# Optimization experiments

Hardware: AMD Instinct MI355X
Metric: run time of the kernel (lower is better)

The kernel has to match this reference:

```python
import jax, jax.numpy as jnp
import numpy as np

T, N, D, FF, H, L, WND = 32, 512, 128, 2048, 8, 2, 8
EPS = 1e-5


def setup_inputs() -> dict:
    key = jax.random.key(0)
    kit = iter(jax.random.split(key, 64))

    def w(shape, scale=0.02):
        return jax.random.normal(next(kit), shape, jnp.float32) * scale

    inp = {"x": jax.random.normal(next(kit), (T, N, D), jnp.float32)}
    # plain transformer encoder (1 layer) params
    inp["enc_in_proj_w"] = w((3 * D, D)); inp["enc_in_proj_b"] = jnp.zeros((3 * D,), jnp.float32)
    inp["enc_out_proj_w"] = w((D, D));    inp["enc_out_proj_b"] = jnp.zeros((D,), jnp.float32)
    inp["enc_lin1_w"] = w((FF, D));       inp["enc_lin1_b"] = jnp.zeros((FF,), jnp.float32)
    inp["enc_lin2_w"] = w((D, FF));       inp["enc_lin2_b"] = jnp.zeros((D,), jnp.float32)
    inp["enc_ln1_w"] = jnp.ones((D,), jnp.float32); inp["enc_ln1_b"] = jnp.zeros((D,), jnp.float32)
    inp["enc_ln2_w"] = jnp.ones((D,), jnp.float32); inp["enc_ln2_b"] = jnp.zeros((D,), jnp.float32)
    # qk transformer encoder (L layers, stacked params)
    inp["qk_in_proj_w"] = w((L, 3 * D, D)); inp["qk_in_proj_b"] = jnp.zeros((L, 3 * D), jnp.float32)
    inp["qk_out_proj_w"] = w((L, D, D));    inp["qk_out_proj_b"] = jnp.zeros((L, D), jnp.float32)
    inp["qk_lin1_w"] = w((L, FF, D));       inp["qk_lin1_b"] = jnp.zeros((L, FF), jnp.float32)
    inp["qk_lin2_w"] = w((L, D, FF));       inp["qk_lin2_b"] = jnp.zeros((L, D), jnp.float32)
    inp["qk_ln1_w"] = jnp.ones((L, D), jnp.float32); inp["qk_ln1_b"] = jnp.zeros((L, D), jnp.float32)
    inp["qk_ln2_w"] = jnp.ones((L, D), jnp.float32); inp["qk_ln2_b"] = jnp.zeros((L, D), jnp.float32)
    # time2vec (SineActivation(1, D))
    inp["t2v_w"] = w((1, D - 1), 1.0); inp["t2v_b"] = w((D - 1,), 1.0)
    inp["t2v_w0"] = w((1, 1), 1.0);    inp["t2v_b0"] = w((1,), 1.0)
    # output head (no bias)
    inp["out_w"] = w((1, D))
    return inp


def _layer_norm(x, g, b):
    m = jnp.mean(x, -1, keepdims=True)
    v = jnp.mean((x - m) ** 2, -1, keepdims=True)
    return (x - m) * jax.lax.rsqrt(v + EPS) * g + b


def _mha(q, k, v, Wi, bi, Wo, bo, mask):
    # q,k,v: [S, B, D] seq-first (torch MultiheadAttention layout)
    S, B, d = q.shape
    dh = d // H
    Wq, Wk, Wv = jnp.split(Wi, 3, axis=0)
    bq, bk, bv = jnp.split(bi, 3, axis=0)
    qh = (q @ Wq.T + bq).reshape(S, B, H, dh)
    kh = (k @ Wk.T + bk).reshape(k.shape[0], B, H, dh)
    vh = (v @ Wv.T + bv).reshape(v.shape[0], B, H, dh)
    scores = jnp.einsum('qbhf,kbhf->bhqk', qh, kh) / np.float32(np.sqrt(dh))
    if mask is not None:
        scores = scores + mask  # additive [S,S] mask broadcast over batch/heads
    a = jax.nn.softmax(scores, axis=-1)
    o = jnp.einsum('bhqk,kbhf->qbhf', a, vh).reshape(S, B, d)
    return o @ Wo.T + bo


def _enc_layer(src, new_v, p, mask):
    # post-LN torch TransformerEncoderLayer (dropout off / eval mode)
    s2 = _mha(src, src, new_v, p['iw'], p['ib'], p['ow'], p['ob'], mask)
    src = _layer_norm(src + s2, p['ln1w'], p['ln1b'])
    h = jax.nn.relu(src @ p['l1w'].T + p['l1b'])
    s2 = h @ p['l2w'].T + p['l2b']
    return _layer_norm(src + s2, p['ln2w'], p['ln2b'])


def _banded_mask():
    # triu(-inf, 1) + triu(-inf, WND).T -> allow i-WND < j <= i
    i = jnp.arange(T)[:, None]
    j = jnp.arange(T)[None, :]
    allowed = (j <= i) & (j > i - WND)
    return jnp.where(allowed, 0.0, -jnp.inf).astype(jnp.float32)


def reference(x, enc_in_proj_w, enc_in_proj_b, enc_out_proj_w, enc_out_proj_b,
              enc_lin1_w, enc_lin1_b, enc_lin2_w, enc_lin2_b,
              enc_ln1_w, enc_ln1_b, enc_ln2_w, enc_ln2_b,
              qk_in_proj_w, qk_in_proj_b, qk_out_proj_w, qk_out_proj_b,
              qk_lin1_w, qk_lin1_b, qk_lin2_w, qk_lin2_b,
              qk_ln1_w, qk_ln1_b, qk_ln2_w, qk_ln2_b,
              t2v_w, t2v_b, t2v_w0, t2v_b0, out_w):
    # 1) plain encoder over the PAIR axis (original transposes before it: seq=N, batch=T)
    xs = jnp.transpose(x, (1, 0, 2))  # [N, T, D]
    p_enc = dict(iw=enc_in_proj_w, ib=enc_in_proj_b, ow=enc_out_proj_w, ob=enc_out_proj_b,
                 l1w=enc_lin1_w, l1b=enc_lin1_b, l2w=enc_lin2_w, l2b=enc_lin2_b,
                 ln1w=enc_ln1_w, ln1b=enc_ln1_b, ln2w=enc_ln2_w, ln2b=enc_ln2_b)
    outs_zs = jnp.transpose(_enc_layer(xs, xs, p_enc, None), (1, 0, 2))  # [T, N, D]
    # 2) time2vec positional signal at tau = 1..T
    tau = jnp.arange(1, T + 1, dtype=jnp.float32)[:, None]  # [T,1]
    t2v = jnp.concatenate([jnp.sin(tau @ t2v_w + t2v_b), tau @ t2v_w0 + t2v_b0], axis=-1)
    out = x + t2v[:, None, :]  # [T, N, D]
    # 3) qk encoder stack with banded causal+window mask, values = outs_zs
    mask = _banded_mask()
    for l in range(L):
        p = dict(iw=qk_in_proj_w[l], ib=qk_in_proj_b[l], ow=qk_out_proj_w[l], ob=qk_out_proj_b[l],
                 l1w=qk_lin1_w[l], l1b=qk_lin1_b[l], l2w=qk_lin2_w[l], l2b=qk_lin2_b[l],
                 ln1w=qk_ln1_w[l], ln1b=qk_ln1_b[l], ln2w=qk_ln2_w[l], ln2b=qk_ln2_b[l])
        out = _enc_layer(out, outs_zs, p, mask)
    return (out @ out_w.T)[..., 0]  # [T, N]
```

## Files before the change

kernel.cpp:

```cpp
#include <hip/hip_runtime.h>
#include <hip/hip_bf16.h>
#include <math.h>

#define TT 32
#define NN 512
#define DD 128
#define FF_ 2048
#define HH 8
#define LL 2
#define WND_ 8
#define TOK (TT*NN)
#define DH 16

typedef __hip_bfloat16 bf16;
typedef __attribute__((ext_vector_type(8))) short bf16x8;
typedef __attribute__((ext_vector_type(4))) float f32x4;

#define GLD_LDS16(gp, lp) __builtin_amdgcn_global_load_lds( \
    (const __attribute__((address_space(1))) unsigned int*)(gp), \
    (__attribute__((address_space(3))) unsigned int*)(lp), 16, 0, 0)

#define MFMA16(a, b, c) __builtin_amdgcn_mfma_f32_16x16x32_bf16((a), (b), (c), 0, 0, 0)

__device__ inline short f2bs(float f) {
    __hip_bfloat16 h = __float2bfloat16(f);
    return *reinterpret_cast<short*>(&h);
}

template<int BM, int BN>
__global__ __launch_bounds__(256) void mfma_gemm(
    const bf16* __restrict__ A, int lda,
    const bf16* __restrict__ W,
    const float* __restrict__ bias,
    bf16* __restrict__ C, int ldc,
    int K, int relu)
{
    constexpr int WM = BM / 2, WN = BN / 2;
    constexpr int FM = WM / 16, FN = WN / 16;
    constexpr int LA = (BM * 64) / (256 * 16);
    constexpr int LB = (BN * 64) / (256 * 16);

    __shared__ bf16 As[BM * 32];
    __shared__ bf16 Bs[BN * 32];

    const int tid  = threadIdx.x;
    const int lane = tid & 63;
    const int wave = tid >> 6;
    const int wm = wave >> 1, wn = wave & 1;
    const int bm = blockIdx.y * BM, bn = blockIdx.x * BN;

    f32x4 acc[FM][FN];
    #pragma unroll
    for (int m = 0; m < FM; m++)
        #pragma unroll
        for (int n = 0; n < FN; n++)
            acc[m][n] = (f32x4){0.f, 0.f, 0.f, 0.f};

    for (int k0 = 0; k0 < K; k0 += 32) {
        #pragma unroll
        for (int i = 0; i < LA; i++) {
            const int o = (tid + i * 256) * 16;
            const int row = o >> 6;
            const int ce  = (o & 63) >> 1;
            GLD_LDS16(A + (size_t)(bm + row) * lda + k0 + ce, (char*)As + o);
        }
        #pragma unroll
        for (int i = 0; i < LB; i++) {
            const int o = (tid + i * 256) * 16;
            const int row = o >> 6;
            const int ce  = (o & 63) >> 1;
            GLD_LDS16(W + (size_t)(bn + row) * K + k0 + ce, (char*)Bs + o);
        }
        __syncthreads();

        bf16x8 af[FM], bfr[FN];
        #pragma unroll
        for (int m = 0; m < FM; m++)
            af[m] = *(const bf16x8*)(As + (wm * WM + m * 16 + (lane & 15)) * 32 + (lane >> 4) * 8);
        #pragma unroll
        for (int n = 0; n < FN; n++)
            bfr[n] = *(const bf16x8*)(Bs + (wn * WN + n * 16 + (lane & 15)) * 32 + (lane >> 4) * 8);
        #pragma unroll
        for (int m = 0; m < FM; m++)
            #pragma unroll
            for (int n = 0; n < FN; n++)
                acc[m][n] = MFMA16(af[m], bfr[n], acc[m][n]);
        __syncthreads();
    }

    #pragma unroll
    for (int n = 0; n < FN; n++) {
        const int col = bn + wn * WN + n * 16 + (lane & 15);
        const float bv = bias[col];
        #pragma unroll
        for (int m = 0; m < FM; m++) {
            #pragma unroll
            for (int r = 0; r < 4; r++) {
                const int row = bm + wm * WM + m * 16 + (lane >> 4) * 4 + r;
                float v = acc[m][n][r] + bv;
                if (relu) v = fmaxf(v, 0.f);
                C[(size_t)row * ldc + col] = __float2bfloat16(v);
            }
        }
    }
}

__global__ __launch_bounds__(256) void mfma_gemm_ln(
    const bf16* __restrict__ A, int lda,
    const bf16* __restrict__ W,
    const float* __restrict__ bias,
    const bf16* __restrict__ R,
    const float* __restrict__ lng, const float* __restrict__ lnb,
    bf16* __restrict__ Y,
    int K)
{
    constexpr int BM = 64, WM = 32, WN = 64, FM = 2, FN = 4;

    __shared__ bf16 As[BM * 32];
    __shared__ bf16 Bs[128 * 32];
    __shared__ float rsum[BM][2];
    __shared__ float rsq[BM][2];

    const int tid  = threadIdx.x;
    const int lane = tid & 63;
    const int wave = tid >> 6;
    const int wm = wave >> 1, wn = wave & 1;
    const int bm = blockIdx.x * BM;

    f32x4 acc[FM][FN];
    #pragma unroll
    for (int m = 0; m < FM; m++)
        #pragma unroll
        for (int n = 0; n < FN; n++)
            acc[m][n] = (f32x4){0.f, 0.f, 0.f, 0.f};

    for (int k0 = 0; k0 < K; k0 += 32) {
        {
            const int o = tid * 16;
            const int row = o >> 6;
            const int ce  = (o & 63) >> 1;
            GLD_LDS16(A + (size_t)(bm + row) * lda + k0 + ce, (char*)As + o);
        }
        #pragma unroll
        for (int i = 0; i < 2; i++) {
            const int o = (tid + i * 256) * 16;
            const int row = o >> 6;
            const int ce  = (o & 63) >> 1;
            GLD_LDS16(W + (size_t)row * K + k0 + ce, (char*)Bs + o);
        }
        __syncthreads();

        bf16x8 af[FM], bfr[FN];
        #pragma unroll
        for (int m = 0; m < FM; m++)
            af[m] = *(const bf16x8*)(As + (wm * WM + m * 16 + (lane & 15)) * 32 + (lane >> 4) * 8);
        #pragma unroll
        for (int n = 0; n < FN; n++)
            bfr[n] = *(const bf16x8*)(Bs + (wn * WN + n * 16 + (lane & 15)) * 32 + (lane >> 4) * 8);
        #pragma unroll
        for (int m = 0; m < FM; m++)
            #pragma unroll
            for (int n = 0; n < FN; n++)
                acc[m][n] = MFMA16(af[m], bfr[n], acc[m][n]);
        __syncthreads();
    }

    #pragma unroll
    for (int n = 0; n < FN; n++) {
        const int col = wn * WN + n * 16 + (lane & 15);
        const float bv = bias[col];
        #pragma unroll
        for (int m = 0; m < FM; m++) {
            #pragma unroll
            for (int r = 0; r < 4; r++) {
                const int rl = wm * WM + m * 16 + (lane >> 4) * 4 + r;
                acc[m][n][r] += bv + __bfloat162float(R[(size_t)(bm + rl) * 128 + col]);
            }
        }
    }

    #pragma unroll
    for (int m = 0; m < FM; m++) {
        #pragma unroll
        for (int r = 0; r < 4; r++) {
            float s = 0.f, q = 0.f;
            #pragma unroll
            for (int n = 0; n < FN; n++) { float v = acc[m][n][r]; s += v; q += v * v; }
            #pragma unroll
            for (int off = 1; off < 16; off <<= 1) {
                s += __shfl_xor(s, off);
                q += __shfl_xor(q, off);
            }
            const int rl = wm * WM + m * 16 + (lane >> 4) * 4 + r;
            if ((lane & 15) == 0) { rsum[rl][wn] = s; rsq[rl][wn] = q; }
        }
    }
    __syncthreads();

    #pragma unroll
    for (int m = 0; m < FM; m++) {
        #pragma unroll
        for (int r = 0; r < 4; r++) {
            const int rl = wm * WM + m * 16 + (lane >> 4) * 4 + r;
            const float S = rsum[rl][0] + rsum[rl][1];
            const float Q = rsq[rl][0] + rsq[rl][1];
            const float mean = S * (1.0f / 128.0f);
            const float var  = Q * (1.0f / 128.0f) - mean * mean;
            const float rstd = rsqrtf(var + 1e-5f);
            #pragma unroll
            for (int n = 0; n < FN; n++) {
                const int col = wn * WN + n * 16 + (lane & 15);
                const float y = (acc[m][n][r] - mean) * rstd * lng[col] + lnb[col];
                Y[(size_t)(bm + rl) * 128 + col] = __float2bfloat16(y);
            }
        }
    }
}

template<bool HEAD>
__global__ __launch_bounds__(512) void ffn_fused(
    const bf16* __restrict__ A,
    const bf16* __restrict__ W1, const float* __restrict__ b1,
    const bf16* __restrict__ W2, const float* __restrict__ b2,
    const float* __restrict__ lng, const float* __restrict__ lnb,
    bf16* __restrict__ Y,
    const float* __restrict__ hw, float* __restrict__ hout)
{
    __shared__ char smem[131072];

    const int tid  = threadIdx.x;
    const int lane = tid & 63;
    const int wv   = tid >> 6;
    const int tg   = wv & 1;
    const int hq   = wv >> 1;
    const int l4   = lane & 15;
    const int g    = lane >> 4;
    const int bm   = blockIdx.x * 64;

    bf16x8 tf[2][4];
    #pragma unroll
    for (int sub = 0; sub < 2; sub++)
        #pragma unroll
        for (int j = 0; j < 4; j++)
            tf[sub][j] = *(const bf16x8*)(A + (size_t)(bm + (tg * 2 + sub) * 16 + l4) * 128
                                          + j * 32 + g * 8);

    const int q    = tid >> 4;
    const int qq   = q & 15;
    const int piq  = (((qq >> 2) << 3) | (qq & 3)) + ((q >> 4) << 2);
    const int w1cb = ((tid & 15) * 16) ^ ((q & 7) << 4);
    const int w2row = tid >> 2;
    const int w2ce  = ((tid & 3) ^ ((w2row >> 1) & 3)) * 8;

    auto STAGE = [&](int d, int s) {
        #pragma unroll
        for (int hx = 0; hx < 4; hx++) {
            const int c0 = hx * 512 + s * 32;
            GLD_LDS16((const char*)W1 + (size_t)(c0 + piq) * 256 + w1cb,
                      smem + d * 32768 + hx * 8192 + tid * 16);
            GLD_LDS16(W2 + (size_t)w2row * 2048 + c0 + w2ce,
                      smem + 65536 + d * 32768 + hx * 8192 + tid * 16);
        }
    };

    f32x4 Oacc[2][8];
    #pragma unroll
    for (int sub = 0; sub < 2; sub++)
        #pragma unroll
        for (int ot = 0; ot < 8; ot++)
            Oacc[sub][ot] = (f32x4){0.f, 0.f, 0.f, 0.f};

    const f32x4 zz = (f32x4){0.f, 0.f, 0.f, 0.f};
    const int xsw = (l4 & 7) << 4;
    const int w2rsw = (l4 >> 1) & 3;

    STAGE(0, 0);
    for (int s = 0; s < 16; s++) {
        __syncthreads();
        if (s < 15) STAGE((s + 1) & 1, s + 1);
        const int d  = s & 1;
        const int c0 = hq * 512 + s * 32;
        const char* w1b = smem + d * 32768 + hq * 8192;
        const char* w2b = smem + 65536 + d * 32768 + hq * 8192;

        f32x4 sa00 = zz, sa01 = zz, sa10 = zz, sa11 = zz;
        #pragma unroll
        for (int j = 0; j < 4; j++) {
            const int xo = (j * 64 + g * 16) ^ xsw;
            bf16x8 w10 = *(const bf16x8*)(w1b + l4 * 256 + xo);
            bf16x8 w11 = *(const bf16x8*)(w1b + (16 + l4) * 256 + xo);
            sa00 = MFMA16(w10, tf[0][j], sa00);
            sa01 = MFMA16(w10, tf[1][j], sa01);
            sa10 = MFMA16(w11, tf[0][j], sa10);
            sa11 = MFMA16(w11, tf[1][j], sa11);
        }
        float4 bv0 = *(const float4*)(b1 + c0 + g * 8);
        float4 bv1 = *(const float4*)(b1 + c0 + g * 8 + 4);
        bf16x8 pf0, pf1;
        pf0[0] = f2bs(fmaxf(sa00[0] + bv0.x, 0.f));
        pf0[1] = f2bs(fmaxf(sa00[1] + bv0.y, 0.f));
        pf0[2] = f2bs(fmaxf(sa00[2] + bv0.z, 0.f));
        pf0[3] = f2bs(fmaxf(sa00[3] + bv0.w, 0.f));
        pf0[4] = f2bs(fmaxf(sa10[0] + bv1.x, 0.f));
        pf0[5] = f2bs(fmaxf(sa10[1] + bv1.y, 0.f));
        pf0[6] = f2bs(fmaxf(sa10[2] + bv1.z, 0.f));
        pf0[7] = f2bs(fmaxf(sa10[3] + bv1.w, 0.f));
        pf1[0] = f2bs(fmaxf(sa01[0] + bv0.x, 0.f));
        pf1[1] = f2bs(fmaxf(sa01[1] + bv0.y, 0.f));
        pf1[2] = f2bs(fmaxf(sa01[2] + bv0.z, 0.f));
        pf1[3] = f2bs(fmaxf(sa01[3] + bv0.w, 0.f));
        pf1[4] = f2bs(fmaxf(sa11[0] + bv1.x, 0.f));
        pf1[5] = f2bs(fmaxf(sa11[1] + bv1.y, 0.f));
        pf1[6] = f2bs(fmaxf(sa11[2] + bv1.z, 0.f));
        pf1[7] = f2bs(fmaxf(sa11[3] + bv1.w, 0.f));

        #pragma unroll
        for (int ot = 0; ot < 8; ot++) {
            bf16x8 w2f = *(const bf16x8*)(w2b + (ot * 16 + l4) * 64 + ((g ^ w2rsw) << 4));
            Oacc[0][ot] = MFMA16(pf0, w2f, Oacc[0][ot]);
            Oacc[1][ot] = MFMA16(pf1, w2f, Oacc[1][ot]);
        }
    }

    __syncthreads();
    if (hq != 0) {
        #pragma unroll
        for (int sub = 0; sub < 2; sub++)
            #pragma unroll
            for (int ot = 0; ot < 8; ot++)
                *(f32x4*)(smem + tg * 49152 + (hq - 1) * 16384 + (sub * 8 + ot) * 1024
                          + lane * 16) = Oacc[sub][ot];
    }
    __syncthreads();
    if (hq == 0) {
        #pragma unroll
        for (int p = 0; p < 3; p++)
            #pragma unroll
            for (int sub = 0; sub < 2; sub++)
                #pragma unroll
                for (int ot = 0; ot < 8; ot++) {
                    f32x4 o2 = *(const f32x4*)(smem + tg * 49152 + p * 16384
                                               + (sub * 8 + ot) * 1024 + lane * 16);
                    Oacc[sub][ot][0] += o2[0]; Oacc[sub][ot][1] += o2[1];
                    Oacc[sub][ot][2] += o2[2]; Oacc[sub][ot][3] += o2[3];
                }

        #pragma unroll
        for (int sub = 0; sub < 2; sub++) {
            float vv[8][4];
            #pragma unroll
            for (int ot = 0; ot < 8; ot++) {
                const int col = ot * 16 + l4;
                const float bv = b2[col];
                #pragma unroll
                for (int r = 0; r < 4; r++) {
                    const int trow = bm + (tg * 2 + sub) * 16 + 4 * g + r;
                    vv[ot][r] = Oacc[sub][ot][r] + bv
                              + __bfloat162float(A[(size_t)trow * 128 + col]);
                }
            }

            #pragma unroll
            for (int r = 0; r < 4; r++) {
                float sm = 0.f, qs = 0.f;
                #pragma unroll
                for (int ot = 0; ot < 8; ot++) { float v = vv[ot][r]; sm += v; qs += v * v; }
                #pragma unroll
                for (int off = 1; off < 16; off <<= 1) {
                    sm += __shfl_xor(sm, off);
                    qs += __shfl_xor(qs, off);
                }
                const float mean = sm * (1.0f / 128.0f);
                const float var  = qs * (1.0f / 128.0f) - mean * mean;
                const float rstd = rsqrtf(var + 1e-5f);
                const int trow = bm + (tg * 2 + sub) * 16 + 4 * g + r;
                float hacc = 0.f;
                #pragma unroll
                for (int ot = 0; ot < 8; ot++) {
                    const int col = ot * 16 + l4;
                    const float y = (vv[ot][r] - mean) * rstd * lng[col] + lnb[col];
                    if (HEAD) hacc += y * hw[col];
                    else Y[(size_t)trow * 128 + col] = __float2bfloat16(y);
                }
                if (HEAD) {
                    #pragma unroll
                    for (int off = 1; off < 16; off <<= 1) hacc += __shfl_xor(hacc, off);
                    if (l4 == 0) hout[trow] = hacc;
                }
            }
        }
    }
}

struct ConvDesc {
    const float *x, *s1, *s2, *s3, *s4, *s5, *s6, *s7, *s8;
    bf16 *dx, *d1, *d2, *d3, *d4, *d5, *d6, *d7, *d8;
    const float *w, *b, *w0, *b0;
    float* tbl;
};

__device__ inline void cvt4(const float* s, bf16* d, int j) {
    float4 v = ((const float4*)s)[j];
    ushort4 o;
    o.x = (unsigned short)f2bs(v.x); o.y = (unsigned short)f2bs(v.y);
    o.z = (unsigned short)f2bs(v.z); o.w = (unsigned short)f2bs(v.w);
    *(ushort4*)((unsigned short*)d + j * 4) = o;
}

#define CP0 524288
#define CP1 536576
#define CP2 540672
#define CP3 606208
#define CP4 671744
#define CP5 696320
#define CP6 704512
#define CP7 835584
#define CP8 966656
#define CP9 967680

__global__ __launch_bounds__(256) void conv_all_kernel(ConvDesc cd)
{
    int i = blockIdx.x * 256 + threadIdx.x;
    if (i < CP0)      cvt4(cd.x,  cd.dx, i);
    else if (i < CP1) cvt4(cd.s1, cd.d1, i - CP0);
    else if (i < CP2) cvt4(cd.s2, cd.d2, i - CP1);
    else if (i < CP3) cvt4(cd.s3, cd.d3, i - CP2);
    else if (i < CP4) cvt4(cd.s4, cd.d4, i - CP3);
    else if (i < CP5) cvt4(cd.s5, cd.d5, i - CP4);
    else if (i < CP6) cvt4(cd.s6, cd.d6, i - CP5);
    else if (i < CP7) cvt4(cd.s7, cd.d7, i - CP6);
    else if (i < CP8) cvt4(cd.s8, cd.d8, i - CP7);
    else if (i < CP9) {
        int e = (i - CP8) * 4;
        int t = e >> 7;
        float tau = (float)(t + 1);
        float4 o;
        #pragma unroll
        for (int k = 0; k < 4; k++) {
            int d = (e + k) & 127;
            ((float*)&o)[k] = (d < 127) ? sinf(tau * cd.w[d] + cd.b[d])
                                        : (tau * cd.w0[0] + cd.b0[0]);
        }
        *(float4*)(cd.tbl + e) = o;
    }
}

__global__ __launch_bounds__(256) void attn_full_mfma(
    const bf16* __restrict__ Qkv, bf16* __restrict__ C)
{
    __shared__ bf16 Qs[512 * 16];
    __shared__ bf16 Ks[512 * 16];
    __shared__ bf16 Vt[16 * 520];
    __shared__ bf16 Zero[32];

    const int t = blockIdx.x >> 3;
    const int h = blockIdx.x & 7;
    const int tid = threadIdx.x;

    if (tid < 32) ((unsigned short*)Zero)[tid] = 0;

    for (int n = tid; n < 512; n += 256) {
        const unsigned short* row = (const unsigned short*)Qkv + (size_t)(t * 512 + n) * 384 + h * 16;
        uint4 q0 = *(const uint4*)(row);
        uint4 q1 = *(const uint4*)(row + 8);
        uint4 k0 = *(const uint4*)(row + 128);
        uint4 k1 = *(const uint4*)(row + 136);
        uint4 v0 = *(const uint4*)(row + 256);
        uint4 v1 = *(const uint4*)(row + 264);
        *(uint4*)((unsigned short*)Qs + n * 16)     = q0;
        *(uint4*)((unsigned short*)Qs + n * 16 + 8) = q1;
        *(uint4*)((unsigned short*)Ks + n * 16)     = k0;
        *(uint4*)((unsigned short*)Ks + n * 16 + 8) = k1;
        union { uint4 u[2]; unsigned short s[16]; } vb;
        vb.u[0] = v0; vb.u[1] = v1;
        #pragma unroll
        for (int f = 0; f < 16; f++)
            ((unsigned short*)Vt)[f * 520 + n] = vb.s[f];
    }
    __syncthreads();

    const int lane = tid & 63;
    const int wv   = tid >> 6;
    const int l4   = lane & 15;
    const int g    = lane >> 4;
    const int qbase = wv * 128;
    const bf16* zp = Zero + (g & 1) * 8;
    const int p0 = ((l4 >> 2) << 3) | (l4 & 3);

    bf16x8 qf[8];
    #pragma unroll
    for (int qt = 0; qt < 8; qt++) {
        const bf16* ap = (g < 2) ? (Qs + (qbase + qt * 16 + l4) * 16 + g * 8) : zp;
        qf[qt] = *(const bf16x8*)ap;
    }

    f32x4 Oacc[8];
    float lsum[8];
    #pragma unroll
    for (int qt = 0; qt < 8; qt++) { Oacc[qt] = (f32x4){0.f,0.f,0.f,0.f}; lsum[qt] = 0.f; }

    const float cexp = 0.25f * 1.44269504088896f;

    for (int kt = 0; kt < 16; kt++) {
        const bf16* k0p = (g < 2) ? (Ks + (kt * 32 + p0)     * 16 + g * 8) : zp;
        const bf16* k1p = (g < 2) ? (Ks + (kt * 32 + p0 + 4) * 16 + g * 8) : zp;
        bf16x8 kf0 = *(const bf16x8*)k0p;
        bf16x8 kf1 = *(const bf16x8*)k1p;
        bf16x8 vf  = *(const bf16x8*)(Vt + l4 * 520 + kt * 32 + g * 8);

        #pragma unroll
        for (int qt = 0; qt < 8; qt++) {
            f32x4 z = (f32x4){0.f,0.f,0.f,0.f};
            f32x4 s0 = MFMA16(kf0, qf[qt], z);
            f32x4 s1 = MFMA16(kf1, qf[qt], z);
            float e[8];
            #pragma unroll
            for (int r = 0; r < 4; r++) {
                e[r]     = exp2f(s0[r] * cexp);
                e[4 + r] = exp2f(s1[r] * cexp);
            }
            lsum[qt] += ((e[0]+e[1])+(e[2]+e[3])) + ((e[4]+e[5])+(e[6]+e[7]));
            bf16x8 pf;
            #pragma unroll
            for (int i = 0; i < 8; i++) pf[i] = f2bs(e[i]);
            Oacc[qt] = MFMA16(pf, vf, Oacc[qt]);
        }
    }

    #pragma unroll
    for (int qt = 0; qt < 8; qt++) {
        float ls = lsum[qt];
        ls += __shfl_xor(ls, 16);
        ls += __shfl_xor(ls, 32);
        #pragma unroll
        for (int r = 0; r < 4; r++) {
            float lq = __shfl(ls, g * 4 + r);
            float o = Oacc[qt][r] / lq;
            int qrow = t * 512 + qbase + qt * 16 + g * 4 + r;
            C[(size_t)qrow * 128 + h * 16 + l4] = __float2bfloat16(o);
        }
    }
}

__global__ __launch_bounds__(256) void attn_banded_kernel(
    const bf16* __restrict__ Qkv, const bf16* __restrict__ Vb, bf16* __restrict__ C)
{
    __shared__ float Qs[TT][129];
    __shared__ float Ksh[TT][129];
    __shared__ float Vs[TT][129];
    const int n = blockIdx.x;
    const int tid = threadIdx.x;

    for (int e = tid; e < TT * DD; e += 256) {
        int t = e >> 7, d = e & 127;
        const bf16* row = Qkv + (size_t)(t * NN + n) * 384;
        Qs[t][d]  = __bfloat162float(row[d]);
        Ksh[t][d] = __bfloat162float(row[128 + d]);
        Vs[t][d]  = __bfloat162float(Vb[(size_t)(t * NN + n) * DD + d]);
    }
    __syncthreads();

    const int h = tid >> 5, i = tid & 31;
    const int hb = h * DH;

    float s[WND_];
    #pragma unroll
    for (int kk = 0; kk < WND_; kk++) {
        int j = i - (WND_ - 1) + kk;
        int jc = j < 0 ? 0 : j;
        float d = 0.f;
        #pragma unroll
        for (int f = 0; f < DH; f++) d += Qs[i][hb + f] * Ksh[jc][hb + f];
        s[kk] = (j >= 0) ? d * 0.25f : -1e30f;
    }
    float m = s[0];
    #pragma unroll
    for (int kk = 1; kk < WND_; kk++) m = fmaxf(m, s[kk]);
    float l = 0.f, p[WND_];
    #pragma unroll
    for (int kk = 0; kk < WND_; kk++) { p[kk] = __expf(s[kk] - m); l += p[kk]; }
    float inv = 1.f / l;
    float acc[DH] = {};
    #pragma unroll
    for (int kk = 0; kk < WND_; kk++) {
        int j = i - (WND_ - 1) + kk;
        int jc = j < 0 ? 0 : j;
        float pw = p[kk] * inv;
        #pragma unroll
        for (int f = 0; f < DH; f++) acc[f] += pw * Vs[jc][hb + f];
    }
    bf16* cp = C + (size_t)(i * NN + n) * DD + hb;
    #pragma unroll
    for (int f = 0; f < DH; f++) cp[f] = __float2bfloat16(acc[f]);
}

__global__ __launch_bounds__(256) void t2v_add_kernel(
    const float* __restrict__ x, const float* __restrict__ tbl, bf16* __restrict__ Y)
{
    int i = blockIdx.x * 256 + threadIdx.x;
    int e = i * 4;
    float4 xv = ((const float4*)x)[i];
    int ti = ((e >> 16) << 7) | (e & 127);
    float4 tv = *(const float4*)(tbl + ti);
    ushort4 o;
    o.x = (unsigned short)f2bs(xv.x + tv.x);
    o.y = (unsigned short)f2bs(xv.y + tv.y);
    o.z = (unsigned short)f2bs(xv.z + tv.z);
    o.w = (unsigned short)f2bs(xv.w + tv.w);
    *(ushort4*)((unsigned short*)Y + e) = o;
}


extern "C" void kernel_launch(void* const* d_in, const int* in_sizes, int n_in,
                              void* d_out, int out_size, void* d_ws, size_t ws_size,
                              hipStream_t stream) {
    const float* x           = (const float*)d_in[0];
    const float* enc_in_w    = (const float*)d_in[1];
    const float* enc_in_b    = (const float*)d_in[2];
    const float* enc_out_w   = (const float*)d_in[3];
    const float* enc_out_b   = (const float*)d_in[4];
    const float* enc_l1w     = (const float*)d_in[5];
    const float* enc_l1b     = (const float*)d_in[6];
    const float* enc_l2w     = (const float*)d_in[7];
    const float* enc_l2b     = (const float*)d_in[8];
    const float* enc_ln1w    = (const float*)d_in[9];
    const float* enc_ln1b    = (const float*)d_in[10];
    const float* enc_ln2w    = (const float*)d_in[11];
    const float* enc_ln2b    = (const float*)d_in[12];
    const float* qk_in_w     = (const float*)d_in[13];
    const float* qk_in_b     = (const float*)d_in[14];
    const float* qk_out_w    = (const float*)d_in[15];
    const float* qk_out_b    = (const float*)d_in[16];
    const float* qk_l1w      = (const float*)d_in[17];
    const float* qk_l1b      = (const float*)d_in[18];
    const float* qk_l2w      = (const float*)d_in[19];
    const float* qk_l2b      = (const float*)d_in[20];
    const float* qk_ln1w     = (const float*)d_in[21];
    const float* qk_ln1b     = (const float*)d_in[22];
    const float* qk_ln2w     = (const float*)d_in[23];
    const float* qk_ln2b     = (const float*)d_in[24];
    const float* t2v_w       = (const float*)d_in[25];
    const float* t2v_b       = (const float*)d_in[26];
    const float* t2v_w0      = (const float*)d_in[27];
    const float* t2v_b0      = (const float*)d_in[28];
    const float* out_w       = (const float*)d_in[29];
    float* out = (float*)d_out;

    char* ws = (char*)d_ws;
    const size_t TOKD = (size_t)TOK * DD;
    size_t off = 0;
    auto alloc = [&](size_t bytes) { char* p = ws + off; off += (bytes + 255) & ~(size_t)255; return p; };

    bf16*  Qb   = (bf16*)alloc((size_t)TOK * 384 * 2);
    bf16*  Vb   = (bf16*)alloc(TOKD * 2);
    bf16*  xb   = (bf16*)alloc(TOKD * 2);
    bf16*  bufA = (bf16*)alloc(TOKD * 2);
    bf16*  Zb   = (bf16*)alloc(TOKD * 2);
    bf16*  Cb   = (bf16*)alloc(TOKD * 2);
    float* t2vt = (float*)alloc((size_t)TT * DD * 4);
    bf16* enc_in_wb  = (bf16*)alloc(384 * DD * 2);
    bf16* enc_out_wb = (bf16*)alloc(DD * DD * 2);
    bf16* enc_l1wb   = (bf16*)alloc((size_t)FF_ * DD * 2);
    bf16* enc_l2wb   = (bf16*)alloc((size_t)DD * FF_ * 2);
    bf16* qk_in_wb   = (bf16*)alloc((size_t)LL * 384 * DD * 2);
    bf16* qk_out_wb  = (bf16*)alloc((size_t)LL * DD * DD * 2);
    bf16* qk_l1wb    = (bf16*)alloc((size_t)LL * FF_ * DD * 2);
    bf16* qk_l2wb    = (bf16*)alloc((size_t)LL * DD * FF_ * 2);

    ConvDesc cd;
    cd.x  = x;        cd.dx = xb;
    cd.s1 = enc_in_w; cd.d1 = enc_in_wb;
    cd.s2 = enc_out_w;cd.d2 = enc_out_wb;
    cd.s3 = enc_l1w;  cd.d3 = enc_l1wb;
    cd.s4 = enc_l2w;  cd.d4 = enc_l2wb;
    cd.s5 = qk_in_w;  cd.d5 = qk_in_wb;
    cd.s6 = qk_out_w; cd.d6 = qk_out_wb;
    cd.s7 = qk_l1w;   cd.d7 = qk_l1wb;
    cd.s8 = qk_l2w;   cd.d8 = qk_l2wb;
    cd.w = t2v_w; cd.b = t2v_b; cd.w0 = t2v_w0; cd.b0 = t2v_b0; cd.tbl = t2vt;
    conv_all_kernel<<<(CP9 + 255) / 256, 256, 0, stream>>>(cd);

    auto gemm128 = [&](const bf16* A, int lda, const bf16* W, const float* bias,
                       bf16* C, int ldc, int M, int N, int K, int relu) {
        dim3 grid(N / 128, M / 128);
        mfma_gemm<128, 128><<<grid, 256, 0, stream>>>(A, lda, W, bias, C, ldc, K, relu);
    };
    auto gemm64 = [&](const bf16* A, int lda, const bf16* W, const float* bias,
                      bf16* C, int ldc, int M, int N, int K, int relu) {
        dim3 grid(N / 64, M / 64);
        mfma_gemm<64, 64><<<grid, 256, 0, stream>>>(A, lda, W, bias, C, ldc, K, relu);
    };
    auto gemm_ln = [&](const bf16* A, int lda, const bf16* W, const float* bias,
                       const bf16* R, const float* lng, const float* lnb,
                       bf16* Y, int M, int K) {
        mfma_gemm_ln<<<M / 64, 256, 0, stream>>>(A, lda, W, bias, R, lng, lnb, Y, K);
    };

    gemm128(xb, DD, enc_in_wb, enc_in_b, Qb, 384, TOK, 384, DD, 0);
    attn_full_mfma<<<TT * HH, 256, 0, stream>>>(Qb, Cb);
    gemm_ln(Cb, DD, enc_out_wb, enc_out_b, xb, enc_ln1w, enc_ln1b, bufA, TOK, DD);
    ffn_fused<false><<<TOK / 64, 512, 0, stream>>>(
        bufA, enc_l1wb, enc_l1b, enc_l2wb, enc_l2b,
        enc_ln2w, enc_ln2b, Zb, nullptr, nullptr);

    t2v_add_kernel<<<(TOK * DD / 4) / 256, 256, 0, stream>>>(x, t2vt, bufA);

    for (int l = 0; l < LL; l++) {
        const bf16* iw   = qk_in_wb  + (size_t)l * 384 * DD;
        const float* ib  = qk_in_b   + (size_t)l * 384;
        const bf16* owt  = qk_out_wb + (size_t)l * DD * DD;
        const float* ob  = qk_out_b  + (size_t)l * DD;
        const bf16* l1w  = qk_l1wb   + (size_t)l * FF_ * DD;
        const float* l1b = qk_l1b    + (size_t)l * FF_;
        const bf16* l2w  = qk_l2wb   + (size_t)l * DD * FF_;
        const float* l2b = qk_l2b    + (size_t)l * DD;

        gemm128(bufA, DD, iw, ib, Qb, 384, TOK, 256, DD, 0);
        gemm64(Zb, DD, iw + (size_t)256 * DD, ib + 256, Vb, DD, TOK, DD, DD, 0);
        attn_banded_kernel<<<NN, 256, 0, stream>>>(Qb, Vb, Cb);
        gemm_ln(Cb, DD, owt, ob, bufA, qk_ln1w + l * DD, qk_ln1b + l * DD, bufA, TOK, DD);
        if (l == LL - 1) {
            ffn_fused<true><<<TOK / 64, 512, 0, stream>>>(
                bufA, l1w, l1b, l2w, l2b,
                qk_ln2w + l * DD, qk_ln2b + l * DD, nullptr, out_w, out);
        } else {
            ffn_fused<false><<<TOK / 64, 512, 0, stream>>>(
                bufA, l1w, l1b, l2w, l2b,
                qk_ln2w + l * DD, qk_ln2b + l * DD, bufA, nullptr, nullptr);
        }
    }
}
```

Before: 222.9 us.

## Fuse QK/V projections into one launch and attention with out-proj+LayerNorm

Merges the Q/K projection and the separate V projection into a single kernel whose third column block reads from the encoder output. It also fuses the banded attention with the output projection, residual add and LayerNorm, so the context stays in swizzled LDS instead of round-tripping through global memory. This removes two kernel launches per layer and the context buffer write and read. The cost is that Wo is read directly from global memory by every block, and the attention blocks now carry more LDS and register pressure.

```diff
diff --git a/kernel.cpp b/kernel.cpp
--- a/kernel.cpp
+++ b/kernel.cpp
@@ -100,6 +100,83 @@
                 float v = acc[m][n][r] + bv;
                 if (relu) v = fmaxf(v, 0.f);
                 C[(size_t)row * ldc + col] = __float2bfloat16(v);
+            }
+        }
+    }
+}
+
+__global__ __launch_bounds__(256) void qkv_proj(
+    const bf16* __restrict__ A1, const bf16* __restrict__ A2,
+    const bf16* __restrict__ W,
+    const float* __restrict__ bias,
+    bf16* __restrict__ Qb, bf16* __restrict__ Vb)
+{
+    constexpr int BM = 128, BN = 128, WM = 64, WN = 64, FM = 4, FN = 4;
+
+    __shared__ bf16 As[BM * 32];
+    __shared__ bf16 Bs[BN * 32];
+
+    const int tid  = threadIdx.x;
+    const int lane = tid & 63;
+    const int wave = tid >> 6;
+    const int wm = wave >> 1, wn = wave & 1;
+    const int bnb = blockIdx.x;
+    const int bm  = blockIdx.y * BM;
+
+    const bf16* A  = (bnb == 2) ? A2 : A1;
+    const bf16* Wb = W + (size_t)bnb * 128 * 128;
+
+    f32x4 acc[FM][FN];
+    #pragma unroll
+    for (int m = 0; m < FM; m++)
+        #pragma unroll
+        for (int n = 0; n < FN; n++)
+            acc[m][n] = (f32x4){0.f, 0.f, 0.f, 0.f};
+
+    for (int k0 = 0; k0 < 128; k0 += 32) {
+        #pragma unroll
+        for (int i = 0; i < 2; i++) {
+            const int o = (tid + i * 256) * 16;
+            const int row = o >> 6;
+            const int ce  = (o & 63) >> 1;
+            GLD_LDS16(A + (size_t)(bm + row) * 128 + k0 + ce, (char*)As + o);
+        }
+        #pragma unroll
+        for (int i = 0; i < 2; i++) {
+            const int o = (tid + i * 256) * 16;
+            const int row = o >> 6;
+            const int ce  = (o & 63) >> 1;
+            GLD_LDS16(Wb + (size_t)row * 128 + k0 + ce, (char*)Bs + o);
+        }
+        __syncthreads();
+
+        bf16x8 af[FM], bfr[FN];
+        #pragma unroll
+        for (int m = 0; m < FM; m++)
+            af[m] = *(const bf16x8*)(As + (wm * WM + m * 16 + (lane & 15)) * 32 + (lane >> 4) * 8);
+        #pragma unroll
+        for (int n = 0; n < FN; n++)
+            bfr[n] = *(const bf16x8*)(Bs + (wn * WN + n * 16 + (lane & 15)) * 32 + (lane >> 4) * 8);
+        #pragma unroll
+        for (int m = 0; m < FM; m++)
+            #pragma unroll
+            for (int n = 0; n < FN; n++)
+                acc[m][n] = MFMA16(af[m], bfr[n], acc[m][n]);
+        __syncthreads();
+    }
+
+    #pragma unroll
+    for (int n = 0; n < FN; n++) {
+        const int cl = wn * WN + n * 16 + (lane & 15);
+        const float bv = bias[bnb * 128 + cl];
+        #pragma unroll
+        for (int m = 0; m < FM; m++) {
+            #pragma unroll
+            for (int r = 0; r < 4; r++) {
+                const int row = bm + wm * WM + m * 16 + (lane >> 4) * 4 + r;
+                const float v = acc[m][n][r] + bv;
+                if (bnb == 2) Vb[(size_t)row * 128 + cl] = __float2bfloat16(v);
+                else          Qb[(size_t)row * 384 + bnb * 128 + cl] = __float2bfloat16(v);
             }
         }
     }
@@ -542,12 +619,22 @@
     }
 }
 
-__global__ __launch_bounds__(256) void attn_banded_kernel(
-    const bf16* __restrict__ Qkv, const bf16* __restrict__ Vb, bf16* __restrict__ C)
+__global__ __launch_bounds__(256) void attn_banded_oln(
+    const bf16* __restrict__ Qkv,
+    const bf16* __restrict__ Vb,
+    const bf16* __restrict__ Wo,
+    const float* __restrict__ ob,
+    const bf16* __restrict__ R,
+    const float* __restrict__ lng, const float* __restrict__ lnb,
+    bf16* __restrict__ Y)
 {
     __shared__ float Qs[TT][129];
     __shared__ float Ksh[TT][129];
     __shared__ float Vs[TT][129];
+    __shared__ bf16 Ctx[32 * 128];
+    __shared__ float rsum[32][2];
+    __shared__ float rsq[32][2];
+
     const int n = blockIdx.x;
     const int tid = threadIdx.x;
 
@@ -560,38 +647,111 @@
     }
     __syncthreads();
 
-    const int h = tid >> 5, i = tid & 31;
-    const int hb = h * DH;
-
-    float s[WND_];
-    #pragma unroll
-    for (int kk = 0; kk < WND_; kk++) {
-        int j = i - (WND_ - 1) + kk;
-        int jc = j < 0 ? 0 : j;
-        float d = 0.f;
-        #pragma unroll
-        for (int f = 0; f < DH; f++) d += Qs[i][hb + f] * Ksh[jc][hb + f];
-        s[kk] = (j >= 0) ? d * 0.25f : -1e30f;
-    }
-    float m = s[0];
-    #pragma unroll
-    for (int kk = 1; kk < WND_; kk++) m = fmaxf(m, s[kk]);
-    float l = 0.f, p[WND_];
-    #pragma unroll
-    for (int kk = 0; kk < WND_; kk++) { p[kk] = __expf(s[kk] - m); l += p[kk]; }
-    float inv = 1.f / l;
-    float acc[DH] = {};
-    #pragma unroll
-    for (int kk = 0; kk < WND_; kk++) {
-        int j = i - (WND_ - 1) + kk;
-        int jc = j < 0 ? 0 : j;
-        float pw = p[kk] * inv;
-        #pragma unroll
-        for (int f = 0; f < DH; f++) acc[f] += pw * Vs[jc][hb + f];
-    }
-    bf16* cp = C + (size_t)(i * NN + n) * DD + hb;
-    #pragma unroll
-    for (int f = 0; f < DH; f++) cp[f] = __float2bfloat16(acc[f]);
+    {
+        const int h = tid >> 5, i = tid & 31;
+        const int hb = h * DH;
+
+        float s[WND_];
+        #pragma unroll
+        for (int kk = 0; kk < WND_; kk++) {
+            int j = i - (WND_ - 1) + kk;
+            int jc = j < 0 ? 0 : j;
+            float d = 0.f;
+            #pragma unroll
+            for (int f = 0; f < DH; f++) d += Qs[i][hb + f] * Ksh[jc][hb + f];
+            s[kk] = (j >= 0) ? d * 0.25f : -1e30f;
+        }
+        float m = s[0];
+        #pragma unroll
+        for (int kk = 1; kk < WND_; kk++) m = fmaxf(m, s[kk]);
+        float l = 0.f, p[WND_];
+        #pragma unroll
+        for (int kk = 0; kk < WND_; kk++) { p[kk] = __expf(s[kk] - m); l += p[kk]; }
+        float inv = 1.f / l;
+        float acc[DH] = {};
+        #pragma unroll
+        for (int kk = 0; kk < WND_; kk++) {
+            int j = i - (WND_ - 1) + kk;
+            int jc = j < 0 ? 0 : j;
+            float pw = p[kk] * inv;
+            #pragma unroll
+            for (int f = 0; f < DH; f++) acc[f] += pw * Vs[jc][hb + f];
+        }
+        union { unsigned short s16[16]; uint4 u[2]; } pk;
+        #pragma unroll
+        for (int f = 0; f < DH; f++) pk.s16[f] = (unsigned short)f2bs(acc[f]);
+        const int base = i * 256 + hb * 2;
+        const int sx = (i & 7) << 4;
+        *(uint4*)((char*)Ctx + ((base)      ^ sx)) = pk.u[0];
+        *(uint4*)((char*)Ctx + ((base + 16) ^ sx)) = pk.u[1];
+    }
+    __syncthreads();
+
+    const int lane = tid & 63;
+    const int wv   = tid >> 6;
+    const int wm = wv >> 1, wn = wv & 1;
+    const int l4 = lane & 15, g = lane >> 4;
+
+    f32x4 acc2[4];
+    #pragma unroll
+    for (int n2 = 0; n2 < 4; n2++) acc2[n2] = (f32x4){0.f, 0.f, 0.f, 0.f};
+
+    const int arow = wm * 16 + l4;
+    const int axor = (arow & 7) << 4;
+    #pragma unroll
+    for (int ks = 0; ks < 4; ks++) {
+        bf16x8 a = *(const bf16x8*)((const char*)Ctx + ((arow * 256 + ks * 64 + g * 16) ^ axor));
+        #pragma unroll
+        for (int n2 = 0; n2 < 4; n2++) {
+            const int col = wn * 64 + n2 * 16 + l4;
+            bf16x8 w = *(const bf16x8*)(Wo + (size_t)col * 128 + ks * 32 + g * 8);
+            acc2[n2] = MFMA16(a, w, acc2[n2]);
+        }
+    }
+
+    float vv[4][4];
+    #pragma unroll
+    for (int n2 = 0; n2 < 4; n2++) {
+        const int col = wn * 64 + n2 * 16 + l4;
+        const float bv = ob[col];
+        #pragma unroll
+        for (int r = 0; r < 4; r++) {
+            const int tloc = wm * 16 + g * 4 + r;
+            vv[n2][r] = acc2[n2][r] + bv
+                      + __bfloat162float(R[(size_t)(tloc * NN + n) * 128 + col]);
+        }
+    }
+
+    #pragma unroll
+    for (int r = 0; r < 4; r++) {
+        float sm = 0.f, qs = 0.f;
+        #pragma unroll
+        for (int n2 = 0; n2 < 4; n2++) { float v = vv[n2][r]; sm += v; qs += v * v; }
+        #pragma unroll
+        for (int off = 1; off < 16; off <<= 1) {
+            sm += __shfl_xor(sm, off);
+            qs += __shfl_xor(qs, off);
+        }
+        const int tloc = wm * 16 + g * 4 + r;
+        if (l4 == 0) { rsum[tloc][wn] = sm; rsq[tloc][wn] = qs; }
+    }
+    __syncthreads();
+
+    #pragma unroll
+    for (int r = 0; r < 4; r++) {
+        const int tloc = wm * 16 + g * 4 + r;
+        const float S = rsum[tloc][0] + rsum[tloc][1];
+        const float Q = rsq[tloc][0] + rsq[tloc][1];
+        const float mean = S * (1.0f / 128.0f);
+        const float var  = Q * (1.0f / 128.0f) - mean * mean;
+        const float rstd = rsqrtf(var + 1e-5f);
+        #pragma unroll
+        for (int n2 = 0; n2 < 4; n2++) {
+            const int col = wn * 64 + n2 * 16 + l4;
+            const float y = (vv[n2][r] - mean) * rstd * lng[col] + lnb[col];
+            Y[(size_t)(tloc * NN + n) * 128 + col] = __float2bfloat16(y);
+        }
+    }
 }
 
 __global__ __launch_bounds__(256) void t2v_add_kernel(
@@ -685,11 +845,6 @@
         dim3 grid(N / 128, M / 128);
         mfma_gemm<128, 128><<<grid, 256, 0, stream>>>(A, lda, W, bias, C, ldc, K, relu);
     };
-    auto gemm64 = [&](const bf16* A, int lda, const bf16* W, const float* bias,
-                      bf16* C, int ldc, int M, int N, int K, int relu) {
-        dim3 grid(N / 64, M / 64);
-        mfma_gemm<64, 64><<<grid, 256, 0, stream>>>(A, lda, W, bias, C, ldc, K, relu);
-    };
     auto gemm_ln = [&](const bf16* A, int lda, const bf16* W, const float* bias,
                        const bf16* R, const float* lng, const float* lnb,
                        bf16* Y, int M, int K) {
@@ -715,10 +870,9 @@
         const bf16* l2w  = qk_l2wb   + (size_t)l * DD * FF_;
         const float* l2b = qk_l2b    + (size_t)l * DD;
 
-        gemm128(bufA, DD, iw, ib, Qb, 384, TOK, 256, DD, 0);
-        gemm64(Zb, DD, iw + (size_t)256 * DD, ib + 256, Vb, DD, TOK, DD, DD, 0);
-        attn_banded_kernel<<<NN, 256, 0, stream>>>(Qb, Vb, Cb);
-        gemm_ln(Cb, DD, owt, ob, bufA, qk_ln1w + l * DD, qk_ln1b + l * DD, bufA, TOK, DD);
+        qkv_proj<<<dim3(3, TOK / 128), 256, 0, stream>>>(bufA, Zb, iw, ib, Qb, Vb);
+        attn_banded_oln<<<NN, 256, 0, stream>>>(Qb, Vb, owt, ob, bufA,
+                                                qk_ln1w + l * DD, qk_ln1b + l * DD, bufA);
         if (l == LL - 1) {
             ffn_fused<true><<<TOK / 64, 512, 0, stream>>>(
                 bufA, l1w, l1b, l2w, l2b,
```

Measured after the change: 215.0 us. 1.04x faster.
